# Optimization experiments

Hardware: AMD Instinct MI355X
Metric: run time of the kernel (lower is better)

## Reference

```python
import jax, jax.numpy as jnp
import numpy as np

N = 50000          # nodes
E = 800000         # edges
D_IN = 768         # LM embedding dim (hardcoded in SimpleHGN first conv)
H = 128            # hidden_dim
REL_DIM = 32       # hardcoded rel_dim
N_REL = 3          # n_relations
BETA = 0.05        # SimpleHGN_att_res
NEG_SLOPE = 0.2    # LeakyReLU in attention


def setup_inputs() -> dict:
    key = jax.random.key(0)
    ks = jax.random.split(key, 16)
    s = 0.05  # param init scale
    return {
        'x': jax.random.normal(ks[0], (N, D_IN), jnp.float32),
        'edge_index': jax.random.randint(ks[1], (2, E), 0, N, dtype=jnp.int64),
        'edge_type': jax.random.randint(ks[2], (E,), 0, N_REL, dtype=jnp.int64),
        'W0': jax.random.normal(ks[3], (D_IN, H), jnp.float32) * s,
        'Wr0': jax.random.normal(ks[4], (REL_DIM, H), jnp.float32) * s,
        'a0': jax.random.normal(ks[5], (3 * H, 1), jnp.float32) * s,
        'rel0': jax.random.normal(ks[6], (N_REL, REL_DIM), jnp.float32) * s,
        'W1': jax.random.normal(ks[7], (H, H), jnp.float32) * s,
        'Wr1': jax.random.normal(ks[8], (REL_DIM, H), jnp.float32) * s,
        'a1': jax.random.normal(ks[9], (3 * H, 1), jnp.float32) * s,
        'rel1': jax.random.normal(ks[10], (N_REL, REL_DIM), jnp.float32) * s,
        'pool_w': jax.random.normal(ks[11], (H, H), jnp.float32) * s,
        'pool_b': jnp.zeros((H,), jnp.float32),
        'out_w': jax.random.normal(ks[12], (H, 2), jnp.float32) * s,
        'out_b': jnp.zeros((2,), jnp.float32),
    }


def _hgn_conv(x, src, dst, et, W, Wr, a, rel, pre_alpha):
    """One SimpleHGNConv layer. Returns (ELU(aggregated), alpha detached)."""
    h = x @ W                                   # [N, H]
    r = rel[et] @ Wr                            # [E, H] edge-type embedding
    aw = a[:, 0]
    a_i, a_j, a_r = aw[:h.shape[1]], aw[h.shape[1]:2 * h.shape[1]], aw[2 * h.shape[1]:]
    # logits = leaky_relu(cat(h_i, h_j, r) @ a) computed without [E,3H] concat
    node_i = h @ a_i                            # [N]
    node_j = h @ a_j                            # [N]
    logit = jax.nn.leaky_relu(node_i[dst] + node_j[src] + r @ a_r, NEG_SLOPE)  # [E]
    # segment softmax over destination node neighborhoods (PyG softmax, +1e-16)
    m = jax.ops.segment_max(logit, dst, num_segments=N)
    e = jnp.exp(logit - m[dst])
    ssum = jax.ops.segment_sum(e, dst, num_segments=N)
    alpha = e / (ssum[dst] + 1e-16)             # [E]
    if pre_alpha is not None:
        alpha = alpha * (1.0 - BETA) + pre_alpha * BETA
    msg = h[src] * alpha[:, None]               # [E, H]
    out = jax.ops.segment_sum(msg, dst, num_segments=N)  # [N, H]
    return jax.nn.elu(out), jax.lax.stop_gradient(alpha)


def reference(x, edge_index, edge_type, W0, Wr0, a0, rel0, W1, Wr1, a1, rel1,
              pool_w, pool_b, out_w, out_b):
    src, dst = edge_index[0], edge_index[1]     # x_j = source, x_i = target
    h, alpha = _hgn_conv(x, src, dst, edge_type, W0, Wr0, a0, rel0, None)
    h, alpha = _hgn_conv(h, src, dst, edge_type, W1, Wr1, a1, rel1, alpha)
    # dropout is identity in eval; activation = relu per config
    h = jax.nn.relu(h @ pool_w + pool_b)
    return h @ out_w + out_b                    # [N, 2]
```

## Files before the change

kernel.cpp:

```cpp
#include <hip/hip_runtime.h>
#include <hip/hip_fp16.h>
#include <cstdint>
#include <cstddef>

#define N_NODES 50000
#define N_EDGES 800000
#define DIN_    768
#define H_DIM   128
#define N_REL   3
#define BETA_F  0.05f
#define SLOPE_F 0.2f

static inline int cdiv(int a, int b) { return (a + b - 1) / b; }

typedef __attribute__((ext_vector_type(8))) short bf16x8;
typedef __attribute__((ext_vector_type(8))) unsigned short u16x8;
typedef __attribute__((ext_vector_type(4))) float f32x4;

__device__ __forceinline__ unsigned short f2bf(float f) {
  unsigned u = __builtin_bit_cast(unsigned, f);
  unsigned r = (u + 0x7fffu + ((u >> 16) & 1u)) >> 16;
  return (unsigned short)r;
}
__device__ __forceinline__ float bf2f(unsigned short h) {
  unsigned u = ((unsigned)h) << 16;
  return __builtin_bit_cast(float, u);
}

__global__ void k_count(const int* __restrict__ dst, int* __restrict__ deg, int E) {
  int e = blockIdx.x * blockDim.x + threadIdx.x;
  if (e < E) atomicAdd(&deg[dst[e]], 1);
}

__global__ __launch_bounds__(256) void k_scan1(const int* __restrict__ deg,
                                               int* __restrict__ part, int n) {
  __shared__ int wsum[4];
  int i = blockIdx.x * 256 + threadIdx.x;
  int lane = threadIdx.x & 63, w = threadIdx.x >> 6;
  int v = (i < n) ? deg[i] : 0;
  #pragma unroll
  for (int d = 32; d > 0; d >>= 1) v += __shfl_xor(v, d);
  if (lane == 0) wsum[w] = v;
  __syncthreads();
  if (threadIdx.x == 0) part[blockIdx.x] = wsum[0] + wsum[1] + wsum[2] + wsum[3];
}

__global__ __launch_bounds__(256) void k_scan2(int* __restrict__ part,
                                               int* __restrict__ off, int nb, int n) {
  __shared__ int sh[256];
  int t = threadIdx.x;
  int v = (t < nb) ? part[t] : 0;
  int incl = v;
  sh[t] = incl;
  __syncthreads();
  #pragma unroll
  for (int d = 1; d < 256; d <<= 1) {
    int u = (t >= d) ? sh[t - d] : 0;
    __syncthreads();
    sh[t] += u;
    __syncthreads();
  }
  incl = sh[t];
  if (t < nb) part[t] = incl - v;
  if (t == nb - 1) off[n] = incl;
}

__global__ __launch_bounds__(256) void k_scan3(const int* __restrict__ deg,
                                               const int* __restrict__ part,
                                               int* __restrict__ off,
                                               int* __restrict__ cur, int n) {
  __shared__ int wsum[4];
  int i = blockIdx.x * 256 + threadIdx.x;
  int lane = threadIdx.x & 63, w = threadIdx.x >> 6;
  int v = (i < n) ? deg[i] : 0;
  int incl = v;
  #pragma unroll
  for (int d = 1; d < 64; d <<= 1) {
    int u = __shfl_up(incl, d);
    if (lane >= d) incl += u;
  }
  if (lane == 63) wsum[w] = incl;
  __syncthreads();
  int woff = 0;
  #pragma unroll
  for (int k = 0; k < 4; ++k) woff += (k < w) ? wsum[k] : 0;
  int ex = incl - v + woff + part[blockIdx.x];
  if (i < n) { off[i] = ex; cur[i] = ex; }
}

__global__ void k_fill(const int* __restrict__ dst, int* __restrict__ cur,
                       int* __restrict__ csr, int E) {
  int e = blockIdx.x * blockDim.x + threadIdx.x;
  if (e < E) {
    int p = atomicAdd(&cur[dst[e]], 1);
    csr[p] = e;
  }
}

__global__ __launch_bounds__(128) void k_relscore(const float* __restrict__ rel,
                                                  const float* __restrict__ Wr,
                                                  const float* __restrict__ a,
                                                  float* __restrict__ rs) {
  __shared__ float red[128];
  int k = threadIdx.x;
  for (int t = 0; t < N_REL; ++t) {
    float p = 0.f;
    #pragma unroll
    for (int j = 0; j < 32; ++j) p += rel[t * 32 + j] * Wr[j * H_DIM + k];
    red[k] = p * a[2 * H_DIM + k];
    __syncthreads();
    for (int s = 64; s > 0; s >>= 1) {
      if (k < s) red[k] += red[k + s];
      __syncthreads();
    }
    if (k == 0) rs[t] = red[0];
    __syncthreads();
  }
}

__global__ void k_prep(const float* __restrict__ W, int K,
                       short* __restrict__ th, short* __restrict__ tl) {
  int id = blockIdx.x * 256 + threadIdx.x;
  if (id >= K * 128) return;
  int k = id >> 7, c = id & 127;
  float w = W[id];
  unsigned short h = f2bf(w);
  unsigned short l = f2bf(w - bf2f(h));
  th[(size_t)c * K + k] = (short)h;
  tl[(size_t)c * K + k] = (short)l;
}

#define BM 64
#define BK 64
template <bool BIASRELU, bool W16>
__global__ __launch_bounds__(256, 3) void k_gemm_mfma(const float* __restrict__ A,
                                                      const short* __restrict__ Bth,
                                                      const short* __restrict__ Btl,
                                                      const float* __restrict__ bias,
                                                      float* __restrict__ C,
                                                      __half* __restrict__ C16,
                                                      int n, int K) {
  __shared__ short Ahi[BM * BK], Alo[BM * BK], Bhi[128 * BK], Blo[128 * BK];
  int t = threadIdx.x;
  int l = t & 63, wid = t >> 6;
  int wr = wid >> 1, wc = wid & 1;
  int lr = l & 15, lk = l >> 4;
  int row0 = blockIdx.x * BM;
  f32x4 acc[2][4];
  #pragma unroll
  for (int m = 0; m < 2; ++m)
    #pragma unroll
    for (int nn = 0; nn < 4; ++nn) acc[m][nn] = (f32x4)(0.f);

  for (int k0 = 0; k0 < K; k0 += BK) {
    #pragma unroll
    for (int i = 0; i < 2; ++i) {
      int gid = i * 256 + t;
      int r = gid >> 3, g = gid & 7;
      int gr = row0 + r;
      float4 v0 = make_float4(0.f, 0.f, 0.f, 0.f);
      float4 v1 = make_float4(0.f, 0.f, 0.f, 0.f);
      if (gr < n) {
        const float* ap = A + (size_t)gr * K + k0 + g * 8;
        v0 = *(const float4*)ap;
        v1 = *(const float4*)(ap + 4);
      }
      float f[8] = {v0.x, v0.y, v0.z, v0.w, v1.x, v1.y, v1.z, v1.w};
      u16x8 hv, lv;
      #pragma unroll
      for (int j = 0; j < 8; ++j) {
        unsigned short h = f2bf(f[j]);
        hv[j] = h;
        lv[j] = f2bf(f[j] - bf2f(h));
      }
      int sg = (g ^ (r & 7)) << 3;
      *(u16x8*)&Ahi[r * BK + sg] = hv;
      *(u16x8*)&Alo[r * BK + sg] = lv;
    }
    #pragma unroll
    for (int i = 0; i < 4; ++i) {
      int gid = i * 256 + t;
      int c = gid >> 3, g = gid & 7;
      u16x8 hv = *(const u16x8*)(Bth + (size_t)c * K + k0 + g * 8);
      u16x8 lv = *(const u16x8*)(Btl + (size_t)c * K + k0 + g * 8);
      int sg = (g ^ (c & 7)) << 3;
      *(u16x8*)&Bhi[c * BK + sg] = hv;
      *(u16x8*)&Blo[c * BK + sg] = lv;
    }
    __syncthreads();
    #pragma unroll
    for (int kk = 0; kk < 2; ++kk) {
      int gbase = kk * 4 + lk;
      bf16x8 ah[2], al[2], bh[4], bl[4];
      #pragma unroll
      for (int m = 0; m < 2; ++m) {
        int r = wr * 32 + m * 16 + lr;
        int idx = r * BK + ((gbase ^ (r & 7)) << 3);
        ah[m] = *(const bf16x8*)&Ahi[idx];
        al[m] = *(const bf16x8*)&Alo[idx];
      }
      #pragma unroll
      for (int nn = 0; nn < 4; ++nn) {
        int c = wc * 64 + nn * 16 + lr;
        int idx = c * BK + ((gbase ^ (c & 7)) << 3);
        bh[nn] = *(const bf16x8*)&Bhi[idx];
        bl[nn] = *(const bf16x8*)&Blo[idx];
      }
      #pragma unroll
      for (int m = 0; m < 2; ++m)
        #pragma unroll
        for (int nn = 0; nn < 4; ++nn) {
          acc[m][nn] = __builtin_amdgcn_mfma_f32_16x16x32_bf16(ah[m], bh[nn], acc[m][nn], 0, 0, 0);
          acc[m][nn] = __builtin_amdgcn_mfma_f32_16x16x32_bf16(ah[m], bl[nn], acc[m][nn], 0, 0, 0);
          acc[m][nn] = __builtin_amdgcn_mfma_f32_16x16x32_bf16(al[m], bh[nn], acc[m][nn], 0, 0, 0);
        }
    }
    __syncthreads();
  }
  #pragma unroll
  for (int m = 0; m < 2; ++m) {
    int rbase = row0 + wr * 32 + m * 16 + lk * 4;
    #pragma unroll
    for (int nn = 0; nn < 4; ++nn) {
      int c = wc * 64 + nn * 16 + lr;
      #pragma unroll
      for (int q = 0; q < 4; ++q) {
        int r = rbase + q;
        if (r < n) {
          float v = acc[m][nn][q];
          if (BIASRELU) {
            v += bias[c];
            v = v > 0.f ? v : 0.f;
          }
          C[(size_t)r * 128 + c] = v;
          if (W16) C16[(size_t)r * 128 + c] = __float2half(v);
        }
      }
    }
  }
}

__global__ __launch_bounds__(256) void k_scores(const float* __restrict__ h,
                                                const float* __restrict__ a,
                                                float* __restrict__ ni,
                                                float* __restrict__ nj, int n) {
  int lane = threadIdx.x & 63;
  int w = threadIdx.x >> 6;
  int row = blockIdx.x * 4 + w;
  if (row >= n) return;
  float2 v = ((const float2*)(h + (size_t)row * H_DIM))[lane];
  float2 ai = ((const float2*)a)[lane];
  float2 aj = ((const float2*)(a + H_DIM))[lane];
  float si = v.x * ai.x + v.y * ai.y;
  float sj = v.x * aj.x + v.y * aj.y;
  #pragma unroll
  for (int d = 32; d > 0; d >>= 1) {
    si += __shfl_xor(si, d);
    sj += __shfl_xor(sj, d);
  }
  if (lane == 0) { ni[row] = si; nj[row] = sj; }
}

__global__ void k_logit(const int* __restrict__ src, const int* __restrict__ dst,
                        const int* __restrict__ et,
                        const float* __restrict__ ni, const float* __restrict__ nj,
                        const float* __restrict__ rs,
                        float* __restrict__ logit, int E) {
  int e = blockIdx.x * blockDim.x + threadIdx.x;
  if (e >= E) return;
  float v = ni[dst[e]] + nj[src[e]] + rs[et[e]];
  logit[e] = v > 0.f ? v : SLOPE_F * v;
}

template <int LAYER>
__global__ __launch_bounds__(128) void k_aggregate(const int* __restrict__ off,
                                                   const int* __restrict__ csr,
                                                   const int* __restrict__ src,
                                                   const float* __restrict__ logit,
                                                   const __half* __restrict__ h16,
                                                   float* __restrict__ alpha_io,
                                                   float* __restrict__ hout, int n) {
  __shared__ float l_red[2];
  __shared__ float l_alpha[128];
  __shared__ int   l_src[128];
  int nid = blockIdx.x;
  int t = threadIdx.x;
  int lane = t & 63;
  int w = t >> 6;
  int start = off[nid];
  int deg = off[nid + 1] - start;
  float hv = 0.f;
  if (deg > 0) {
    float m = -INFINITY;
    for (int k = t; k < deg; k += 128) m = fmaxf(m, logit[csr[start + k]]);
    #pragma unroll
    for (int d = 32; d > 0; d >>= 1) m = fmaxf(m, __shfl_xor(m, d));
    if (lane == 0) l_red[w] = m;
    __syncthreads();
    m = fmaxf(l_red[0], l_red[1]);
    __syncthreads();
    float s = 0.f;
    for (int k = t; k < deg; k += 128) s += expf(logit[csr[start + k]] - m);
    #pragma unroll
    for (int d = 32; d > 0; d >>= 1) s += __shfl_xor(s, d);
    if (lane == 0) l_red[w] = s;
    __syncthreads();
    float denom = l_red[0] + l_red[1] + 1e-16f;
    for (int base = 0; base < deg; base += 128) {
      int kk = base + t;
      if (kk < deg) {
        int e = csr[start + kk];
        float al = expf(logit[e] - m) / denom;
        if (LAYER == 1) {
          al = al * (1.f - BETA_F) + BETA_F * alpha_io[e];
        } else {
          alpha_io[e] = al;
        }
        l_alpha[t] = al;
        l_src[t] = src[e];
      }
      __syncthreads();
      int cnt = deg - base; if (cnt > 128) cnt = 128;
      #pragma unroll 4
      for (int k = 0; k < cnt; ++k)
        hv += l_alpha[k] * __half2float(h16[(size_t)l_src[k] * H_DIM + t]);
      __syncthreads();
    }
  }
  hout[(size_t)nid * H_DIM + t] = hv > 0.f ? hv : expm1f(hv);
}

__global__ __launch_bounds__(256) void k_out(const float* __restrict__ P,
                                             const float* __restrict__ ow,
                                             const float* __restrict__ ob,
                                             float* __restrict__ out, int n) {
  int lane = threadIdx.x & 63;
  int w = threadIdx.x >> 6;
  int row = blockIdx.x * 4 + w;
  if (row >= n) return;
  float2 v  = ((const float2*)(P + (size_t)row * H_DIM))[lane];
  float2 w0 = ((const float2*)ow)[2 * lane];
  float2 w1 = ((const float2*)ow)[2 * lane + 1];
  float s0 = v.x * w0.x + v.y * w1.x;
  float s1 = v.x * w0.y + v.y * w1.y;
  #pragma unroll
  for (int d = 32; d > 0; d >>= 1) {
    s0 += __shfl_xor(s0, d);
    s1 += __shfl_xor(s1, d);
  }
  if (lane == 0) {
    out[row * 2]     = s0 + ob[0];
    out[row * 2 + 1] = s1 + ob[1];
  }
}

extern "C" void kernel_launch(void* const* d_in, const int* in_sizes, int n_in,
                              void* d_out, int out_size, void* d_ws, size_t ws_size,
                              hipStream_t stream) {
  const float* x      = (const float*)d_in[0];
  const int*   ei     = (const int*)d_in[1];
  const int*   et     = (const int*)d_in[2];
  const float* W0     = (const float*)d_in[3];
  const float* Wr0    = (const float*)d_in[4];
  const float* a0     = (const float*)d_in[5];
  const float* rel0   = (const float*)d_in[6];
  const float* W1     = (const float*)d_in[7];
  const float* Wr1    = (const float*)d_in[8];
  const float* a1     = (const float*)d_in[9];
  const float* rel1   = (const float*)d_in[10];
  const float* pool_w = (const float*)d_in[11];
  const float* pool_b = (const float*)d_in[12];
  const float* out_w  = (const float*)d_in[13];
  const float* out_b  = (const float*)d_in[14];

  const int* src = ei;
  const int* dst = ei + N_EDGES;

  char* p = (char*)d_ws;
  auto take = [&](size_t bytes) {
    char* r = p;
    p += (bytes + 511) & ~(size_t)511;
    return r;
  };
  int*   deg    = (int*)take((size_t)N_NODES * 4);
  int*   off    = (int*)take((size_t)(N_NODES + 1) * 4);
  int*   cur    = (int*)take((size_t)N_NODES * 4);
  int*   part   = (int*)take((size_t)256 * 4);
  int*   csr    = (int*)take((size_t)N_EDGES * 4);
  float* logit  = (float*)take((size_t)N_EDGES * 4);
  float* alpha0 = (float*)take((size_t)N_EDGES * 4);
  float* ni     = (float*)take((size_t)N_NODES * 4);
  float* nj     = (float*)take((size_t)N_NODES * 4);
  float* rs     = (float*)take(256);
  short* wt0h   = (short*)take((size_t)DIN_ * 128 * 2);
  short* wt0l   = (short*)take((size_t)DIN_ * 128 * 2);
  short* wt1h   = (short*)take((size_t)128 * 128 * 2);
  short* wt1l   = (short*)take((size_t)128 * 128 * 2);
  short* wph    = (short*)take((size_t)128 * 128 * 2);
  short* wpl    = (short*)take((size_t)128 * 128 * 2);
  float* big1   = (float*)take((size_t)N_NODES * H_DIM * 4);
  float* big2   = (float*)take((size_t)N_NODES * H_DIM * 4);
  __half* h16   = (__half*)take((size_t)N_NODES * H_DIM * 2);

  const int EB = cdiv(N_EDGES, 256);
  const int GB = cdiv(N_NODES, BM);
  const int SB = cdiv(N_NODES, 256);

  hipMemsetAsync(deg, 0, (size_t)N_NODES * 4, stream);
  k_count<<<EB, 256, 0, stream>>>(dst, deg, N_EDGES);
  k_scan1<<<SB, 256, 0, stream>>>(deg, part, N_NODES);
  k_scan2<<<1, 256, 0, stream>>>(part, off, SB, N_NODES);
  k_scan3<<<SB, 256, 0, stream>>>(deg, part, off, cur, N_NODES);
  k_fill<<<EB, 256, 0, stream>>>(dst, cur, csr, N_EDGES);

  k_prep<<<cdiv(DIN_ * 128, 256), 256, 0, stream>>>(W0, DIN_, wt0h, wt0l);
  k_prep<<<cdiv(128 * 128, 256), 256, 0, stream>>>(W1, 128, wt1h, wt1l);
  k_prep<<<cdiv(128 * 128, 256), 256, 0, stream>>>(pool_w, 128, wph, wpl);

  k_relscore<<<1, 128, 0, stream>>>(rel0, Wr0, a0, rs);
  k_gemm_mfma<false, true><<<GB, 256, 0, stream>>>(x, wt0h, wt0l, nullptr, big1, h16, N_NODES, DIN_);
  k_scores<<<cdiv(N_NODES, 4), 256, 0, stream>>>(big1, a0, ni, nj, N_NODES);
  k_logit<<<EB, 256, 0, stream>>>(src, dst, et, ni, nj, rs, logit, N_EDGES);
  k_aggregate<0><<<N_NODES, 128, 0, stream>>>(off, csr, src, logit, h16, alpha0, big2, N_NODES);

  k_relscore<<<1, 128, 0, stream>>>(rel1, Wr1, a1, rs);
  k_gemm_mfma<false, true><<<GB, 256, 0, stream>>>(big2, wt1h, wt1l, nullptr, big1, h16, N_NODES, 128);
  k_scores<<<cdiv(N_NODES, 4), 256, 0, stream>>>(big1, a1, ni, nj, N_NODES);
  k_logit<<<EB, 256, 0, stream>>>(src, dst, et, ni, nj, rs, logit, N_EDGES);
  k_aggregate<1><<<N_NODES, 128, 0, stream>>>(off, csr, src, logit, h16, alpha0, big2, N_NODES);

  k_gemm_mfma<true, false><<<GB, 256, 0, stream>>>(big2, wph, wpl, pool_b, big1, nullptr, N_NODES, 128);
  k_out<<<cdiv(N_NODES, 4), 256, 0, stream>>>(big1, out_w, out_b, (float*)d_out, N_NODES);
}
```

Before: 401.0 us.

## Double-buffer GEMM LDS tiles with register prefetch and padded plane layout

Restructures the split-bf16 MFMA GEMM to use a 32-wide K tile with two LDS buffers. The next tile's global loads go into registers while the current tile's MFMAs run, and one barrier per iteration replaces two. The LDS layout changes from XOR swizzling to k-group planes with padding to avoid bank conflicts. The trade-off is more register use for the prefetch values and more, smaller iterations.

```diff
diff --git a/kernel.cpp b/kernel.cpp
--- a/kernel.cpp
+++ b/kernel.cpp
@@ -130,8 +130,13 @@
   tl[(size_t)c * K + k] = (short)l;
 }
 
-#define BM 64
-#define BK 64
+#define A_PLANE 1088
+#define A_ARR   (4 * A_PLANE)
+#define B_PLANE 2112
+#define B_ARR   (4 * B_PLANE)
+#define B_BASE  (4 * A_ARR)
+#define SM_TOT  (B_BASE + 4 * B_ARR)
+
 template <bool BIASRELU, bool W16>
 __global__ __launch_bounds__(256, 3) void k_gemm_mfma(const float* __restrict__ A,
                                                       const short* __restrict__ Bth,
@@ -140,71 +145,96 @@
                                                       float* __restrict__ C,
                                                       __half* __restrict__ C16,
                                                       int n, int K) {
-  __shared__ short Ahi[BM * BK], Alo[BM * BK], Bhi[128 * BK], Blo[128 * BK];
+  __shared__ __align__(16) char sm[SM_TOT];
   int t = threadIdx.x;
   int l = t & 63, wid = t >> 6;
   int wr = wid >> 1, wc = wid & 1;
   int lr = l & 15, lk = l >> 4;
-  int row0 = blockIdx.x * BM;
+  int row0 = blockIdx.x * 64;
+
+  int ar = t >> 2, ag = t & 3;
+  int bc0 = t >> 2,          bg0 = t & 3;
+  int bc1 = (256 + t) >> 2,  bg1 = (256 + t) & 3;
+  int gar = row0 + ar;
+  const float* aptr = (gar < n) ? (A + (size_t)gar * K + ag * 8) : nullptr;
+  const short* bh0p = Bth + (size_t)bc0 * K + bg0 * 8;
+  const short* bh1p = Bth + (size_t)bc1 * K + bg1 * 8;
+  const short* bl0p = Btl + (size_t)bc0 * K + bg0 * 8;
+  const short* bl1p = Btl + (size_t)bc1 * K + bg1 * 8;
+
   f32x4 acc[2][4];
   #pragma unroll
   for (int m = 0; m < 2; ++m)
     #pragma unroll
     for (int nn = 0; nn < 4; ++nn) acc[m][nn] = (f32x4)(0.f);
 
-  for (int k0 = 0; k0 < K; k0 += BK) {
-    #pragma unroll
-    for (int i = 0; i < 2; ++i) {
-      int gid = i * 256 + t;
-      int r = gid >> 3, g = gid & 7;
-      int gr = row0 + r;
-      float4 v0 = make_float4(0.f, 0.f, 0.f, 0.f);
-      float4 v1 = make_float4(0.f, 0.f, 0.f, 0.f);
-      if (gr < n) {
-        const float* ap = A + (size_t)gr * K + k0 + g * 8;
-        v0 = *(const float4*)ap;
-        v1 = *(const float4*)(ap + 4);
-      }
-      float f[8] = {v0.x, v0.y, v0.z, v0.w, v1.x, v1.y, v1.z, v1.w};
-      u16x8 hv, lv;
-      #pragma unroll
-      for (int j = 0; j < 8; ++j) {
-        unsigned short h = f2bf(f[j]);
-        hv[j] = h;
-        lv[j] = f2bf(f[j] - bf2f(h));
-      }
-      int sg = (g ^ (r & 7)) << 3;
-      *(u16x8*)&Ahi[r * BK + sg] = hv;
-      *(u16x8*)&Alo[r * BK + sg] = lv;
-    }
-    #pragma unroll
-    for (int i = 0; i < 4; ++i) {
-      int gid = i * 256 + t;
-      int c = gid >> 3, g = gid & 7;
-      u16x8 hv = *(const u16x8*)(Bth + (size_t)c * K + k0 + g * 8);
-      u16x8 lv = *(const u16x8*)(Btl + (size_t)c * K + k0 + g * 8);
-      int sg = (g ^ (c & 7)) << 3;
-      *(u16x8*)&Bhi[c * BK + sg] = hv;
-      *(u16x8*)&Blo[c * BK + sg] = lv;
-    }
-    __syncthreads();
-    #pragma unroll
-    for (int kk = 0; kk < 2; ++kk) {
-      int gbase = kk * 4 + lk;
+  float4 pa0, pa1;
+  u16x8 pbh0, pbh1, pbl0, pbl1;
+
+  const int nt = K >> 5;
+
+  auto load_tile = [&](int it) {
+    int k0 = it << 5;
+    if (aptr) {
+      pa0 = *(const float4*)(aptr + k0);
+      pa1 = *(const float4*)(aptr + k0 + 4);
+    } else {
+      pa0 = make_float4(0.f, 0.f, 0.f, 0.f);
+      pa1 = make_float4(0.f, 0.f, 0.f, 0.f);
+    }
+    pbh0 = *(const u16x8*)(bh0p + k0);
+    pbh1 = *(const u16x8*)(bh1p + k0);
+    pbl0 = *(const u16x8*)(bl0p + k0);
+    pbl1 = *(const u16x8*)(bl1p + k0);
+  };
+
+  auto write_tile = [&](int buf) {
+    float f[8] = {pa0.x, pa0.y, pa0.z, pa0.w, pa1.x, pa1.y, pa1.z, pa1.w};
+    u16x8 hv, lv;
+    #pragma unroll
+    for (int j = 0; j < 8; ++j) {
+      unsigned short h = f2bf(f[j]);
+      hv[j] = h;
+      lv[j] = f2bf(f[j] - bf2f(h));
+    }
+    char* aH = sm + (buf * 2 + 0) * A_ARR + ag * A_PLANE + ar * 16;
+    char* aL = sm + (buf * 2 + 1) * A_ARR + ag * A_PLANE + ar * 16;
+    *(u16x8*)aH = hv;
+    *(u16x8*)aL = lv;
+    char* bH = sm + B_BASE + (buf * 2 + 0) * B_ARR;
+    char* bL = sm + B_BASE + (buf * 2 + 1) * B_ARR;
+    *(u16x8*)(bH + bg0 * B_PLANE + bc0 * 16) = pbh0;
+    *(u16x8*)(bH + bg1 * B_PLANE + bc1 * 16) = pbh1;
+    *(u16x8*)(bL + bg0 * B_PLANE + bc0 * 16) = pbl0;
+    *(u16x8*)(bL + bg1 * B_PLANE + bc1 * 16) = pbl1;
+  };
+
+  load_tile(0);
+  write_tile(0);
+  __syncthreads();
+
+  int cur = 0;
+  for (int it = 0; it < nt; ++it) {
+    bool more = (it + 1 < nt);
+    if (more) load_tile(it + 1);
+
+    {
+      const char* aH = sm + (cur * 2 + 0) * A_ARR + lk * A_PLANE;
+      const char* aL = sm + (cur * 2 + 1) * A_ARR + lk * A_PLANE;
+      const char* bH = sm + B_BASE + (cur * 2 + 0) * B_ARR + lk * B_PLANE;
+      const char* bL = sm + B_BASE + (cur * 2 + 1) * B_ARR + lk * B_PLANE;
       bf16x8 ah[2], al[2], bh[4], bl[4];
       #pragma unroll
       for (int m = 0; m < 2; ++m) {
         int r = wr * 32 + m * 16 + lr;
-        int idx = r * BK + ((gbase ^ (r & 7)) << 3);
-        ah[m] = *(const bf16x8*)&Ahi[idx];
-        al[m] = *(const bf16x8*)&Alo[idx];
+        ah[m] = *(const bf16x8*)(aH + r * 16);
+        al[m] = *(const bf16x8*)(aL + r * 16);
       }
       #pragma unroll
       for (int nn = 0; nn < 4; ++nn) {
         int c = wc * 64 + nn * 16 + lr;
-        int idx = c * BK + ((gbase ^ (c & 7)) << 3);
-        bh[nn] = *(const bf16x8*)&Bhi[idx];
-        bl[nn] = *(const bf16x8*)&Blo[idx];
+        bh[nn] = *(const bf16x8*)(bH + c * 16);
+        bl[nn] = *(const bf16x8*)(bL + c * 16);
       }
       #pragma unroll
       for (int m = 0; m < 2; ++m)
@@ -215,8 +245,12 @@
           acc[m][nn] = __builtin_amdgcn_mfma_f32_16x16x32_bf16(al[m], bh[nn], acc[m][nn], 0, 0, 0);
         }
     }
-    __syncthreads();
-  }
+
+    if (more) write_tile(cur ^ 1);
+    __syncthreads();
+    cur ^= 1;
+  }
+
   #pragma unroll
   for (int m = 0; m < 2; ++m) {
     int rbase = row0 + wr * 32 + m * 16 + lk * 4;
@@ -403,7 +437,7 @@
   __half* h16   = (__half*)take((size_t)N_NODES * H_DIM * 2);
 
   const int EB = cdiv(N_EDGES, 256);
-  const int GB = cdiv(N_NODES, BM);
+  const int GB = cdiv(N_NODES, 64);
   const int SB = cdiv(N_NODES, 256);
 
   hipMemsetAsync(deg, 0, (size_t)N_NODES * 4, stream);
```

New measurement: 416.6 us. 1.04x slower.

## Load GEMM tiles directly to LDS and pre-swizzle weight splits

Applied to the files above, without the earlier changes.

The MFMA GEMM now stages A as raw fp32 and B hi/lo bf16 tiles straight from global memory into LDS using global_load_lds. This bypasses the register round-trip and the per-element bf16 split during staging. The weight prep kernel writes B already in the tiled, XOR-swizzled LDS layout so it can be copied linearly. The A hi/lo split moves to after the LDS read, and hi now truncates instead of rounding. This cuts staging instructions and VGPR pressure, but each wave now repeats the split work, and the A tile in LDS doubles in size because it stays fp32.

```diff
diff --git a/kernel.cpp b/kernel.cpp
--- a/kernel.cpp
+++ b/kernel.cpp
@@ -26,6 +26,10 @@
   unsigned u = ((unsigned)h) << 16;
   return __builtin_bit_cast(float, u);
 }
+
+#define GLOAD_LDS16(g, s) __builtin_amdgcn_global_load_lds( \
+    (const __attribute__((address_space(1))) void*)(g),      \
+    (__attribute__((address_space(3))) void*)(s), 16, 0, 0)
 
 __global__ void k_count(const int* __restrict__ dst, int* __restrict__ deg, int E) {
   int e = blockIdx.x * blockDim.x + threadIdx.x;
@@ -126,85 +130,101 @@
   float w = W[id];
   unsigned short h = f2bf(w);
   unsigned short l = f2bf(w - bf2f(h));
-  th[(size_t)c * K + k] = (short)h;
-  tl[(size_t)c * K + k] = (short)l;
-}
-
-#define BM 64
-#define BK 64
+  int kt = k >> 6;
+  int g = (k >> 3) & 7;
+  int j = k & 7;
+  int p = g ^ (c & 7);
+  size_t pos = ((size_t)(kt * 128 + c) << 6) + (p << 3) + j;
+  th[pos] = (short)h;
+  tl[pos] = (short)l;
+}
+
 template <bool BIASRELU, bool W16>
 __global__ __launch_bounds__(256, 3) void k_gemm_mfma(const float* __restrict__ A,
-                                                      const short* __restrict__ Bth,
-                                                      const short* __restrict__ Btl,
+                                                      const short* __restrict__ Bswh,
+                                                      const short* __restrict__ Bswl,
                                                       const float* __restrict__ bias,
                                                       float* __restrict__ C,
                                                       __half* __restrict__ C16,
                                                       int n, int K) {
-  __shared__ short Ahi[BM * BK], Alo[BM * BK], Bhi[128 * BK], Blo[128 * BK];
+  __shared__ __align__(16) char Asm[16384];
+  __shared__ __align__(16) char Bhs[16384];
+  __shared__ __align__(16) char Bls[16384];
   int t = threadIdx.x;
   int l = t & 63, wid = t >> 6;
   int wr = wid >> 1, wc = wid & 1;
   int lr = l & 15, lk = l >> 4;
-  int row0 = blockIdx.x * BM;
+  int row0 = blockIdx.x * 64;
+
   f32x4 acc[2][4];
   #pragma unroll
   for (int m = 0; m < 2; ++m)
     #pragma unroll
     for (int nn = 0; nn < 4; ++nn) acc[m][nn] = (f32x4)(0.f);
 
-  for (int k0 = 0; k0 < K; k0 += BK) {
-    #pragma unroll
-    for (int i = 0; i < 2; ++i) {
-      int gid = i * 256 + t;
-      int r = gid >> 3, g = gid & 7;
-      int gr = row0 + r;
-      float4 v0 = make_float4(0.f, 0.f, 0.f, 0.f);
-      float4 v1 = make_float4(0.f, 0.f, 0.f, 0.f);
-      if (gr < n) {
-        const float* ap = A + (size_t)gr * K + k0 + g * 8;
-        v0 = *(const float4*)ap;
-        v1 = *(const float4*)(ap + 4);
-      }
-      float f[8] = {v0.x, v0.y, v0.z, v0.w, v1.x, v1.y, v1.z, v1.w};
-      u16x8 hv, lv;
-      #pragma unroll
-      for (int j = 0; j < 8; ++j) {
-        unsigned short h = f2bf(f[j]);
-        hv[j] = h;
-        lv[j] = f2bf(f[j] - bf2f(h));
-      }
-      int sg = (g ^ (r & 7)) << 3;
-      *(u16x8*)&Ahi[r * BK + sg] = hv;
-      *(u16x8*)&Alo[r * BK + sg] = lv;
-    }
+  const int nt = K >> 6;
+
+  int a_r[4], a_gl[4];
+  #pragma unroll
+  for (int i = 0; i < 4; ++i) {
+    int id = (wid * 4 + i) * 64 + l;
+    int r = id >> 4, s = id & 15;
+    int p32 = s >> 1, b = s & 1;
+    a_r[i] = r;
+    a_gl[i] = (((p32 ^ (r & 7)) << 1) | b);
+  }
+
+  for (int it = 0; it < nt; ++it) {
+    int k0 = it << 6;
     #pragma unroll
     for (int i = 0; i < 4; ++i) {
-      int gid = i * 256 + t;
-      int c = gid >> 3, g = gid & 7;
-      u16x8 hv = *(const u16x8*)(Bth + (size_t)c * K + k0 + g * 8);
-      u16x8 lv = *(const u16x8*)(Btl + (size_t)c * K + k0 + g * 8);
-      int sg = (g ^ (c & 7)) << 3;
-      *(u16x8*)&Bhi[c * BK + sg] = hv;
-      *(u16x8*)&Blo[c * BK + sg] = lv;
-    }
-    __syncthreads();
+      int gr = row0 + a_r[i]; if (gr >= n) gr = n - 1;
+      const float* src = A + (size_t)gr * K + k0 + a_gl[i] * 4;
+      GLOAD_LDS16(src, Asm + (wid * 4 + i) * 1024);
+    }
+    const short* bh_t = Bswh + (size_t)it * 8192;
+    const short* bl_t = Bswl + (size_t)it * 8192;
+    #pragma unroll
+    for (int i = 0; i < 4; ++i) {
+      int id = (wid * 4 + i) * 64 + l;
+      GLOAD_LDS16(bh_t + id * 8, Bhs + (wid * 4 + i) * 1024);
+    }
+    #pragma unroll
+    for (int i = 0; i < 4; ++i) {
+      int id = (wid * 4 + i) * 64 + l;
+      GLOAD_LDS16(bl_t + id * 8, Bls + (wid * 4 + i) * 1024);
+    }
+    __syncthreads();
+
     #pragma unroll
     for (int kk = 0; kk < 2; ++kk) {
-      int gbase = kk * 4 + lk;
-      bf16x8 ah[2], al[2], bh[4], bl[4];
+      int q = kk * 4 + lk;
+      bf16x8 ah[2], al[2];
       #pragma unroll
       for (int m = 0; m < 2; ++m) {
         int r = wr * 32 + m * 16 + lr;
-        int idx = r * BK + ((gbase ^ (r & 7)) << 3);
-        ah[m] = *(const bf16x8*)&Ahi[idx];
-        al[m] = *(const bf16x8*)&Alo[idx];
+        const char* ap = Asm + r * 256 + ((q ^ (r & 7)) << 5);
+        float4 f0 = *(const float4*)ap;
+        float4 f1 = *(const float4*)(ap + 16);
+        float ff[8] = {f0.x, f0.y, f0.z, f0.w, f1.x, f1.y, f1.z, f1.w};
+        u16x8 hv, lv;
+        #pragma unroll
+        for (int j = 0; j < 8; ++j) {
+          unsigned u = __builtin_bit_cast(unsigned, ff[j]);
+          unsigned short h = (unsigned short)(u >> 16);
+          hv[j] = h;
+          lv[j] = f2bf(ff[j] - bf2f(h));
+        }
+        ah[m] = __builtin_bit_cast(bf16x8, hv);
+        al[m] = __builtin_bit_cast(bf16x8, lv);
       }
+      bf16x8 bh[4], bl[4];
       #pragma unroll
       for (int nn = 0; nn < 4; ++nn) {
         int c = wc * 64 + nn * 16 + lr;
-        int idx = c * BK + ((gbase ^ (c & 7)) << 3);
-        bh[nn] = *(const bf16x8*)&Bhi[idx];
-        bl[nn] = *(const bf16x8*)&Blo[idx];
+        int p = q ^ (c & 7);
+        bh[nn] = *(const bf16x8*)(Bhs + c * 128 + p * 16);
+        bl[nn] = *(const bf16x8*)(Bls + c * 128 + p * 16);
       }
       #pragma unroll
       for (int m = 0; m < 2; ++m)
@@ -217,6 +237,7 @@
     }
     __syncthreads();
   }
+
   #pragma unroll
   for (int m = 0; m < 2; ++m) {
     int rbase = row0 + wr * 32 + m * 16 + lk * 4;
@@ -403,7 +424,7 @@
   __half* h16   = (__half*)take((size_t)N_NODES * H_DIM * 2);
 
   const int EB = cdiv(N_EDGES, 256);
-  const int GB = cdiv(N_NODES, BM);
+  const int GB = cdiv(N_NODES, 64);
   const int SB = cdiv(N_NODES, 256);
 
   hipMemsetAsync(deg, 0, (size_t)N_NODES * 4, stream);
```

Result: no change. 395.1 us (-1.5%).

## Load GEMM operands straight into MFMA registers, dropping LDS staging

Applied to the files above, without the earlier changes.

The split-bf16 MFMA GEMM no longer stages A and B tiles through shared memory with barriers. Each lane loads its own A row fragment and B column fragment from global memory and feeds them directly to the MFMA instructions, unrolled by two over K. The bf16 high part of A is now taken by truncation instead of round-to-nearest, with the residual still captured in the low part. This removes LDS traffic and synchronisation, but A rows are loaded in strided 32-byte pieces and B fragments are re-read from global or cache by every wave with no LDS reuse.

```diff
diff --git a/kernel.cpp b/kernel.cpp
--- a/kernel.cpp
+++ b/kernel.cpp
@@ -130,93 +130,85 @@
   tl[(size_t)c * K + k] = (short)l;
 }
 
-#define BM 64
-#define BK 64
 template <bool BIASRELU, bool W16>
-__global__ __launch_bounds__(256, 3) void k_gemm_mfma(const float* __restrict__ A,
-                                                      const short* __restrict__ Bth,
-                                                      const short* __restrict__ Btl,
-                                                      const float* __restrict__ bias,
-                                                      float* __restrict__ C,
-                                                      __half* __restrict__ C16,
-                                                      int n, int K) {
-  __shared__ short Ahi[BM * BK], Alo[BM * BK], Bhi[128 * BK], Blo[128 * BK];
+__global__ __launch_bounds__(256) void k_gemm_direct(const float* __restrict__ A,
+                                                     const short* __restrict__ Bth,
+                                                     const short* __restrict__ Btl,
+                                                     const float* __restrict__ bias,
+                                                     float* __restrict__ C,
+                                                     __half* __restrict__ C16,
+                                                     int n, int K) {
   int t = threadIdx.x;
   int l = t & 63, wid = t >> 6;
   int wr = wid >> 1, wc = wid & 1;
   int lr = l & 15, lk = l >> 4;
-  int row0 = blockIdx.x * BM;
+  int row0 = blockIdx.x * 64;
+
   f32x4 acc[2][4];
   #pragma unroll
   for (int m = 0; m < 2; ++m)
     #pragma unroll
     for (int nn = 0; nn < 4; ++nn) acc[m][nn] = (f32x4)(0.f);
 
-  for (int k0 = 0; k0 < K; k0 += BK) {
-    #pragma unroll
-    for (int i = 0; i < 2; ++i) {
-      int gid = i * 256 + t;
-      int r = gid >> 3, g = gid & 7;
-      int gr = row0 + r;
-      float4 v0 = make_float4(0.f, 0.f, 0.f, 0.f);
-      float4 v1 = make_float4(0.f, 0.f, 0.f, 0.f);
-      if (gr < n) {
-        const float* ap = A + (size_t)gr * K + k0 + g * 8;
-        v0 = *(const float4*)ap;
-        v1 = *(const float4*)(ap + 4);
+  int r0 = row0 + wr * 32 + lr;
+  int r1 = r0 + 16;
+  if (r0 >= n) r0 = n - 1;
+  if (r1 >= n) r1 = n - 1;
+  const float* a0p = A + (size_t)r0 * K + lk * 8;
+  const float* a1p = A + (size_t)r1 * K + lk * 8;
+  const short* bhp[4];
+  const short* blp[4];
+  #pragma unroll
+  for (int nn = 0; nn < 4; ++nn) {
+    int c = wc * 64 + nn * 16 + lr;
+    bhp[nn] = Bth + (size_t)c * K + lk * 8;
+    blp[nn] = Btl + (size_t)c * K + lk * 8;
+  }
+
+  #pragma unroll 2
+  for (int k0 = 0; k0 < K; k0 += 32) {
+    float4 fa00 = *(const float4*)(a0p + k0);
+    float4 fa01 = *(const float4*)(a0p + k0 + 4);
+    float4 fa10 = *(const float4*)(a1p + k0);
+    float4 fa11 = *(const float4*)(a1p + k0 + 4);
+    bf16x8 bh[4], bl[4];
+    #pragma unroll
+    for (int nn = 0; nn < 4; ++nn) {
+      bh[nn] = *(const bf16x8*)(bhp[nn] + k0);
+      bl[nn] = *(const bf16x8*)(blp[nn] + k0);
+    }
+    bf16x8 ah[2], al[2];
+    #pragma unroll
+    for (int m = 0; m < 2; ++m) {
+      float ff[8];
+      if (m == 0) {
+        ff[0]=fa00.x; ff[1]=fa00.y; ff[2]=fa00.z; ff[3]=fa00.w;
+        ff[4]=fa01.x; ff[5]=fa01.y; ff[6]=fa01.z; ff[7]=fa01.w;
+      } else {
+        ff[0]=fa10.x; ff[1]=fa10.y; ff[2]=fa10.z; ff[3]=fa10.w;
+        ff[4]=fa11.x; ff[5]=fa11.y; ff[6]=fa11.z; ff[7]=fa11.w;
       }
-      float f[8] = {v0.x, v0.y, v0.z, v0.w, v1.x, v1.y, v1.z, v1.w};
       u16x8 hv, lv;
       #pragma unroll
       for (int j = 0; j < 8; ++j) {
-        unsigned short h = f2bf(f[j]);
+        unsigned u = __builtin_bit_cast(unsigned, ff[j]);
+        unsigned short h = (unsigned short)(u >> 16);
         hv[j] = h;
-        lv[j] = f2bf(f[j] - bf2f(h));
+        lv[j] = f2bf(ff[j] - bf2f(h));
       }
-      int sg = (g ^ (r & 7)) << 3;
-      *(u16x8*)&Ahi[r * BK + sg] = hv;
-      *(u16x8*)&Alo[r * BK + sg] = lv;
+      ah[m] = __builtin_bit_cast(bf16x8, hv);
+      al[m] = __builtin_bit_cast(bf16x8, lv);
     }
     #pragma unroll
-    for (int i = 0; i < 4; ++i) {
-      int gid = i * 256 + t;
-      int c = gid >> 3, g = gid & 7;
-      u16x8 hv = *(const u16x8*)(Bth + (size_t)c * K + k0 + g * 8);
-      u16x8 lv = *(const u16x8*)(Btl + (size_t)c * K + k0 + g * 8);
-      int sg = (g ^ (c & 7)) << 3;
-      *(u16x8*)&Bhi[c * BK + sg] = hv;
-      *(u16x8*)&Blo[c * BK + sg] = lv;
-    }
-    __syncthreads();
-    #pragma unroll
-    for (int kk = 0; kk < 2; ++kk) {
-      int gbase = kk * 4 + lk;
-      bf16x8 ah[2], al[2], bh[4], bl[4];
-      #pragma unroll
-      for (int m = 0; m < 2; ++m) {
-        int r = wr * 32 + m * 16 + lr;
-        int idx = r * BK + ((gbase ^ (r & 7)) << 3);
-        ah[m] = *(const bf16x8*)&Ahi[idx];
-        al[m] = *(const bf16x8*)&Alo[idx];
-      }
+    for (int m = 0; m < 2; ++m)
       #pragma unroll
       for (int nn = 0; nn < 4; ++nn) {
-        int c = wc * 64 + nn * 16 + lr;
-        int idx = c * BK + ((gbase ^ (c & 7)) << 3);
-        bh[nn] = *(const bf16x8*)&Bhi[idx];
-        bl[nn] = *(const bf16x8*)&Blo[idx];
+        acc[m][nn] = __builtin_amdgcn_mfma_f32_16x16x32_bf16(ah[m], bh[nn], acc[m][nn], 0, 0, 0);
+        acc[m][nn] = __builtin_amdgcn_mfma_f32_16x16x32_bf16(ah[m], bl[nn], acc[m][nn], 0, 0, 0);
+        acc[m][nn] = __builtin_amdgcn_mfma_f32_16x16x32_bf16(al[m], bh[nn], acc[m][nn], 0, 0, 0);
       }
-      #pragma unroll
-      for (int m = 0; m < 2; ++m)
-        #pragma unroll
-        for (int nn = 0; nn < 4; ++nn) {
-          acc[m][nn] = __builtin_amdgcn_mfma_f32_16x16x32_bf16(ah[m], bh[nn], acc[m][nn], 0, 0, 0);
-          acc[m][nn] = __builtin_amdgcn_mfma_f32_16x16x32_bf16(ah[m], bl[nn], acc[m][nn], 0, 0, 0);
-          acc[m][nn] = __builtin_amdgcn_mfma_f32_16x16x32_bf16(al[m], bh[nn], acc[m][nn], 0, 0, 0);
-        }
-    }
-    __syncthreads();
-  }
+  }
+
   #pragma unroll
   for (int m = 0; m < 2; ++m) {
     int rbase = row0 + wr * 32 + m * 16 + lk * 4;
@@ -403,7 +395,7 @@
   __half* h16   = (__half*)take((size_t)N_NODES * H_DIM * 2);
 
   const int EB = cdiv(N_EDGES, 256);
-  const int GB = cdiv(N_NODES, BM);
+  const int GB = cdiv(N_NODES, 64);
   const int SB = cdiv(N_NODES, 256);
 
   hipMemsetAsync(deg, 0, (size_t)N_NODES * 4, stream);
@@ -418,17 +410,17 @@
   k_prep<<<cdiv(128 * 128, 256), 256, 0, stream>>>(pool_w, 128, wph, wpl);
 
   k_relscore<<<1, 128, 0, stream>>>(rel0, Wr0, a0, rs);
-  k_gemm_mfma<false, true><<<GB, 256, 0, stream>>>(x, wt0h, wt0l, nullptr, big1, h16, N_NODES, DIN_);
+  k_gemm_direct<false, true><<<GB, 256, 0, stream>>>(x, wt0h, wt0l, nullptr, big1, h16, N_NODES, DIN_);
   k_scores<<<cdiv(N_NODES, 4), 256, 0, stream>>>(big1, a0, ni, nj, N_NODES);
   k_logit<<<EB, 256, 0, stream>>>(src, dst, et, ni, nj, rs, logit, N_EDGES);
   k_aggregate<0><<<N_NODES, 128, 0, stream>>>(off, csr, src, logit, h16, alpha0, big2, N_NODES);
 
   k_relscore<<<1, 128, 0, stream>>>(rel1, Wr1, a1, rs);
-  k_gemm_mfma<false, true><<<GB, 256, 0, stream>>>(big2, wt1h, wt1l, nullptr, big1, h16, N_NODES, 128);
+  k_gemm_direct<false, true><<<GB, 256, 0, stream>>>(big2, wt1h, wt1l, nullptr, big1, h16, N_NODES, 128);
   k_scores<<<cdiv(N_NODES, 4), 256, 0, stream>>>(big1, a1, ni, nj, N_NODES);
   k_logit<<<EB, 256, 0, stream>>>(src, dst, et, ni, nj, rs, logit, N_EDGES);
   k_aggregate<1><<<N_NODES, 128, 0, stream>>>(off, csr, src, logit, h16, alpha0, big2, N_NODES);
 
-  k_gemm_mfma<true, false><<<GB, 256, 0, stream>>>(big2, wph, wpl, pool_b, big1, nullptr, N_NODES, 128);
+  k_gemm_direct<true, false><<<GB, 256, 0, stream>>>(big2, wph, wpl, pool_b, big1, nullptr, N_NODES, 128);
   k_out<<<cdiv(N_NODES, 4), 256, 0, stream>>>(big1, out_w, out_b, (float*)d_out, N_NODES);
 }
```

Measured after the change: 501.3 us. +25.0%, slower.
